# Kernel optimization log

Hardware: AMD Instinct MI355X
Metric: run time of the kernel (lower is better)

Reference implementation:

```python
import jax, jax.numpy as jnp
import numpy as np

N, E = 100000, 1600000
IN, HID, EMB = 128, 256, 64


def setup_inputs() -> dict:
    key = jax.random.key(0)
    ks = jax.random.split(key, 8)
    x = jax.random.normal(ks[0], (N, IN), dtype=jnp.float32)
    edge_index = jax.random.randint(ks[1], (2, E), 0, N, dtype=jnp.int64)
    def glorot(k, fan_in, fan_out):
        lim = np.sqrt(6.0 / (fan_in + fan_out)).astype(np.float32)
        return jax.random.uniform(k, (fan_in, fan_out), jnp.float32, -lim, lim)
    return {
        "x": x,
        "edge_index": edge_index,
        "W1": glorot(ks[2], IN, HID), "b1": jnp.zeros((HID,), jnp.float32),
        "W2": glorot(ks[3], HID, HID), "b2": jnp.zeros((HID,), jnp.float32),
        "W3": glorot(ks[4], HID, EMB), "b3": jnp.zeros((EMB,), jnp.float32),
    }


def reference(x, edge_index, W1, b1, W2, b2, W3, b3):
    n = x.shape[0]
    # add self loops (PyG GCNConv default, fill_value=1)
    loops = jnp.arange(n, dtype=edge_index.dtype)
    src = jnp.concatenate([edge_index[0], loops])
    dst = jnp.concatenate([edge_index[1], loops])
    # symmetric normalization D^-1/2 A_hat D^-1/2 (degree at target)
    deg = jax.ops.segment_sum(jnp.ones_like(src, dtype=x.dtype), dst, num_segments=n)
    dinv = jnp.where(deg > 0, deg ** -0.5, 0.0)
    norm = (dinv[src] * dinv[dst])[:, None]  # [E+N, 1]

    def conv(h, W, b):
        h = h @ W                               # [N, out]
        agg = jax.ops.segment_sum(h[src] * norm, dst, num_segments=n)
        return agg + b

    h = jax.nn.relu(conv(x, W1, b1))   # dropout: identity in eval mode
    h = jax.nn.relu(conv(h, W2, b2))
    h = conv(h, W3, b3)
    # L2-normalize rows (F.normalize, eps=1e-12)
    nrm = jnp.linalg.norm(h, axis=1, keepdims=True)
    return h / jnp.maximum(nrm, 1e-12)
```

## Files before the change

kernel.cpp:

```cpp
#include <hip/hip_runtime.h>
#include <cstddef>
#include <cstdint>

constexpr int IN_F  = 128;
constexpr int HID_F = 256;
constexpr int EMB_F = 64;

typedef float  f32x4  __attribute__((ext_vector_type(4)));
typedef short  bf16x8 __attribute__((ext_vector_type(8)));
typedef unsigned short ushort_t;
typedef ushort_t u16x8 __attribute__((ext_vector_type(8)));
typedef ushort_t u16x4 __attribute__((ext_vector_type(4)));

__device__ inline float bf2f(ushort_t u) {
  union { unsigned i; float f; } c; c.i = ((unsigned)u) << 16; return c.f;
}
__device__ inline ushort_t f2bf(float f) {
  union { float f; unsigned i; } c; c.f = f;
  unsigned r = c.i + 0x7FFFu + ((c.i >> 16) & 1u);
  return (ushort_t)(r >> 16);
}

constexpr int NBKT = 512;
constexpr int CHUNK = 16384;


__global__ void k_setup(const float* __restrict__ W1, const float* __restrict__ W2,
                        const float* __restrict__ W3,
                        ushort_t* __restrict__ W1t, ushort_t* __restrict__ W2t,
                        ushort_t* __restrict__ W3t, int* __restrict__ ghist) {
  constexpr int c1 = IN_F * HID_F;
  constexpr int c2 = c1 + HID_F * HID_F;
  constexpr int c3 = c2 + HID_F * EMB_F;
  int i = blockIdx.x * blockDim.x + threadIdx.x;
  if (i < c1) {
    int k = i / HID_F, nn = i - k * HID_F;
    W1t[(size_t)nn * IN_F + k] = f2bf(W1[i]);
  } else if (i < c2) {
    int j = i - c1;
    int k = j / HID_F, nn = j - k * HID_F;
    W2t[(size_t)nn * HID_F + k] = f2bf(W2[j]);
  } else if (i < c3) {
    int j = i - c2;
    int k = j / EMB_F, nn = j - k * EMB_F;
    W3t[(size_t)nn * HID_F + k] = f2bf(W3[j]);
  } else if (i - c3 < NBKT) {
    ghist[i - c3] = 0;
  }
}


__global__ __launch_bounds__(512) void k_hist(const int* __restrict__ dst,
                                              int* __restrict__ ghist, int e) {
  __shared__ int cnt[NBKT];
  cnt[threadIdx.x] = 0;
  __syncthreads();
  int i0 = blockIdx.x * CHUNK;
  int i1 = min(e, i0 + CHUNK);
  for (int i = i0 + threadIdx.x; i < i1; i += 512)
    atomicAdd(&cnt[dst[i] >> 8], 1);
  __syncthreads();
  int c = cnt[threadIdx.x];
  if (c > 0) atomicAdd(&ghist[threadIdx.x], c);
}

__global__ __launch_bounds__(512) void k_bscan(const int* __restrict__ ghist,
                                               int* __restrict__ bstart,
                                               int* __restrict__ gcursor) {
  __shared__ int s[NBKT];
  int v = ghist[threadIdx.x];
  s[threadIdx.x] = v;
  __syncthreads();
#pragma unroll
  for (int off = 1; off < NBKT; off <<= 1) {
    int t = (threadIdx.x >= off) ? s[threadIdx.x - off] : 0;
    __syncthreads();
    s[threadIdx.x] += t;
    __syncthreads();
  }
  int ex = s[threadIdx.x] - v;
  bstart[threadIdx.x] = ex;
  gcursor[threadIdx.x] = ex;
}

__global__ __launch_bounds__(512) void k_passA(const int* __restrict__ src,
                                               const int* __restrict__ dst,
                                               int* __restrict__ gcursor,
                                               unsigned* __restrict__ staged, int e) {
  __shared__ int cnt[NBKT];
  __shared__ int base[NBKT];
  cnt[threadIdx.x] = 0;
  __syncthreads();
  int i0 = blockIdx.x * CHUNK;
  int i1 = min(e, i0 + CHUNK);
  for (int i = i0 + threadIdx.x; i < i1; i += 512)
    atomicAdd(&cnt[dst[i] >> 8], 1);
  __syncthreads();
  int c = cnt[threadIdx.x];
  base[threadIdx.x] = (c > 0) ? atomicAdd(&gcursor[threadIdx.x], c) : 0;
  cnt[threadIdx.x] = 0;
  __syncthreads();
  for (int i = i0 + threadIdx.x; i < i1; i += 512) {
    int d = dst[i];
    int b = d >> 8;
    int lp = atomicAdd(&cnt[b], 1);
    staged[base[b] + lp] = ((unsigned)(d & 255) << 17) | (unsigned)src[i];
  }
}

__global__ __launch_bounds__(256) void k_B1scan(const unsigned* __restrict__ staged,
                                                const int* __restrict__ bstart,
                                                const int* __restrict__ ghist,
                                                float* __restrict__ dinv,
                                                int* __restrict__ rowptr,
                                                int* __restrict__ bsum, int n) {
  __shared__ int cnt[256];
  __shared__ int s[256];
  cnt[threadIdx.x] = 0;
  __syncthreads();
  int b = blockIdx.x;
  int beg = bstart[b], end = beg + ghist[b];
  for (int i = beg + threadIdx.x; i < end; i += 256)
    atomicAdd(&cnt[staged[i] >> 17], 1);
  __syncthreads();
  int node = (b << 8) + threadIdx.x;
  int v = (node < n) ? cnt[threadIdx.x] : 0;
  if (node < n) dinv[node] = rsqrtf((float)(v + 1));
  s[threadIdx.x] = v;
  __syncthreads();
#pragma unroll
  for (int off = 1; off < 256; off <<= 1) {
    int t = (threadIdx.x >= off) ? s[threadIdx.x - off] : 0;
    __syncthreads();
    s[threadIdx.x] += t;
    __syncthreads();
  }
  if (node < n) rowptr[node] = s[threadIdx.x] - v;
  if (threadIdx.x == 255) bsum[b] = s[255];
}

__global__ void k_scan2(int* __restrict__ bsum, int nb) {
  __shared__ int s[512];
  int v = (threadIdx.x < nb) ? bsum[threadIdx.x] : 0;
  s[threadIdx.x] = v;
  __syncthreads();
#pragma unroll
  for (int off = 1; off < 512; off <<= 1) {
    int t = (threadIdx.x >= off) ? s[threadIdx.x - off] : 0;
    __syncthreads();
    s[threadIdx.x] += t;
    __syncthreads();
  }
  if (threadIdx.x < nb) bsum[threadIdx.x] = s[threadIdx.x] - v;
}

__global__ void k_scan3x(int* __restrict__ rowptr, const int* __restrict__ bsum,
                         const float* __restrict__ x, const float* __restrict__ dinv,
                         ushort_t* __restrict__ xb, int n, int e) {
  int i = blockIdx.x * blockDim.x + threadIdx.x;
  int n32 = n * 32;
  if (i < n32) {
    float s = dinv[i >> 5];
    float4 v = reinterpret_cast<const float4*>(x)[i];
    u16x4 o;
    o[0] = f2bf(v.x * s); o[1] = f2bf(v.y * s); o[2] = f2bf(v.z * s); o[3] = f2bf(v.w * s);
    reinterpret_cast<u16x4*>(xb)[i] = o;
  } else {
    int j = i - n32;
    if (j < n) rowptr[j] += bsum[j >> 8];
    else if (j == n) rowptr[n] = e;
  }
}

__global__ __launch_bounds__(256) void k_B2(const unsigned* __restrict__ staged,
                                            const int* __restrict__ bstart,
                                            const int* __restrict__ ghist,
                                            const int* __restrict__ rowptr,
                                            int* __restrict__ csr, int n) {
  __shared__ int cur[256];
  cur[threadIdx.x] = 0;
  __syncthreads();
  int b = blockIdx.x;
  int beg = bstart[b], end = beg + ghist[b];
  int nb0 = b << 8;
  for (int i = beg + threadIdx.x; i < end; i += 256) {
    unsigned p = staged[i];
    int l = (int)(p >> 17);
    int s = (int)(p & 0x1FFFFu);
    int pos = rowptr[nb0 + l] + atomicAdd(&cur[l], 1);
    csr[pos] = s;
  }
}


__global__ __launch_bounds__(256) void k_gather1(
    const ushort_t* __restrict__ t, ushort_t* __restrict__ outp,
    const int* __restrict__ rowptr, const int* __restrict__ csr, int n) {
  int wid = (blockIdx.x * blockDim.x + threadIdx.x) >> 6;
  int lane = threadIdx.x & 63;
  if (wid >= n) return;
  const int half = lane >> 5, sub = lane & 31;
  const int coff = sub * 4;
  int beg = rowptr[wid], end = rowptr[wid + 1];
  int nitems = end - beg + 1;
  float acc[4] = {};
  int i = 0;
  for (; i + 3 < nitems; i += 4) {
    int i0 = i + half, i1 = i + 2 + half;
    int r0 = (i0 == 0) ? wid : csr[beg + i0 - 1];
    int r1 = csr[beg + i1 - 1];
    u16x4 v0 = *reinterpret_cast<const u16x4*>(t + (size_t)r0 * IN_F + coff);
    u16x4 v1 = *reinterpret_cast<const u16x4*>(t + (size_t)r1 * IN_F + coff);
#pragma unroll
    for (int k = 0; k < 4; ++k) acc[k] += bf2f(v0[k]);
#pragma unroll
    for (int k = 0; k < 4; ++k) acc[k] += bf2f(v1[k]);
  }
  for (; i < nitems; i += 2) {
    int i0 = i + half;
    if (i0 < nitems) {
      int r0 = (i0 == 0) ? wid : csr[beg + i0 - 1];
      u16x4 v0 = *reinterpret_cast<const u16x4*>(t + (size_t)r0 * IN_F + coff);
#pragma unroll
      for (int k = 0; k < 4; ++k) acc[k] += bf2f(v0[k]);
    }
  }
#pragma unroll
  for (int k = 0; k < 4; ++k) acc[k] += __shfl_xor(acc[k], 32);
  if (half == 0) {
    u16x4 o;
#pragma unroll
    for (int k = 0; k < 4; ++k) o[k] = f2bf(acc[k]);
    *reinterpret_cast<u16x4*>(outp + (size_t)wid * IN_F + coff) = o;
  }
}

__global__ __launch_bounds__(256) void k_gather2(
    const ushort_t* __restrict__ t, ushort_t* __restrict__ outp,
    const int* __restrict__ rowptr, const int* __restrict__ csr,
    const float* __restrict__ dinv, const float* __restrict__ bias, int n) {
  int wid = (blockIdx.x * blockDim.x + threadIdx.x) >> 6;
  int lane = threadIdx.x & 63;
  if (wid >= n) return;
  const int half = lane >> 5, sub = lane & 31;
  const int coff = sub * 8;
  int beg = rowptr[wid], end = rowptr[wid + 1];
  int nitems = end - beg + 1;
  float acc[8] = {};
  int i = 0;
  for (; i + 3 < nitems; i += 4) {
    int i0 = i + half, i1 = i + 2 + half;
    int r0 = (i0 == 0) ? wid : csr[beg + i0 - 1];
    int r1 = csr[beg + i1 - 1];
    u16x8 v0 = *reinterpret_cast<const u16x8*>(t + (size_t)r0 * HID_F + coff);
    u16x8 v1 = *reinterpret_cast<const u16x8*>(t + (size_t)r1 * HID_F + coff);
#pragma unroll
    for (int k = 0; k < 8; ++k) acc[k] += bf2f(v0[k]);
#pragma unroll
    for (int k = 0; k < 8; ++k) acc[k] += bf2f(v1[k]);
  }
  for (; i < nitems; i += 2) {
    int i0 = i + half;
    if (i0 < nitems) {
      int r0 = (i0 == 0) ? wid : csr[beg + i0 - 1];
      u16x8 v0 = *reinterpret_cast<const u16x8*>(t + (size_t)r0 * HID_F + coff);
#pragma unroll
      for (int k = 0; k < 8; ++k) acc[k] += bf2f(v0[k]);
    }
  }
#pragma unroll
  for (int k = 0; k < 8; ++k) acc[k] += __shfl_xor(acc[k], 32);
  if (half == 0) {
    float s = dinv[wid];
    u16x8 o;
#pragma unroll
    for (int k = 0; k < 8; ++k) o[k] = f2bf(fmaxf(fmaf(acc[k], s, bias[coff + k]), 0.f));
    *reinterpret_cast<u16x8*>(outp + (size_t)wid * HID_F + coff) = o;
  }
}

__global__ __launch_bounds__(256) void k_gather3(
    const ushort_t* __restrict__ t, float* __restrict__ outp,
    const int* __restrict__ rowptr, const int* __restrict__ csr,
    const float* __restrict__ dinv, const float* __restrict__ b3, int n) {
  int wid = (blockIdx.x * blockDim.x + threadIdx.x) >> 6;
  int lane = threadIdx.x & 63;
  if (wid >= n) return;
  const int q = lane >> 4, sub = lane & 15;
  const int coff = sub * 4;
  int beg = rowptr[wid], end = rowptr[wid + 1];
  int nitems = end - beg + 1;
  float acc[4] = {};
  for (int i = 0; i < nitems; i += 4) {
    int i0 = i + q;
    if (i0 < nitems) {
      int r0 = (i0 == 0) ? wid : csr[beg + i0 - 1];
      u16x4 v0 = *reinterpret_cast<const u16x4*>(t + (size_t)r0 * EMB_F + coff);
#pragma unroll
      for (int k = 0; k < 4; ++k) acc[k] += bf2f(v0[k]);
    }
  }
#pragma unroll
  for (int k = 0; k < 4; ++k) acc[k] += __shfl_xor(acc[k], 16);
#pragma unroll
  for (int k = 0; k < 4; ++k) acc[k] += __shfl_xor(acc[k], 32);
  float s = dinv[wid];
  float v[4], ss = 0.f;
#pragma unroll
  for (int k = 0; k < 4; ++k) {
    v[k] = fmaf(acc[k], s, b3[coff + k]);
    ss = fmaf(v[k], v[k], ss);
  }
#pragma unroll
  for (int off = 8; off > 0; off >>= 1) ss += __shfl_xor(ss, off);
  float inv = 1.0f / fmaxf(sqrtf(ss), 1e-12f);
  if (lane < 16) {
    float4 o = make_float4(v[0] * inv, v[1] * inv, v[2] * inv, v[3] * inv);
    *reinterpret_cast<float4*>(outp + (size_t)wid * EMB_F + coff) = o;
  }
}


template<int K, bool RELU>
__global__ __launch_bounds__(256) void k_mfma_gemm(
    const ushort_t* __restrict__ A, const ushort_t* __restrict__ Wt,
    ushort_t* __restrict__ C,
    const float* __restrict__ dinv, const float* __restrict__ bias,
    int M, int NT ) {
  int w = blockIdx.x * 4 + (threadIdx.x >> 6);
  int lane = threadIdx.x & 63;
  int mt = w / NT, nt = w - mt * NT;
  int mbase = mt * 64, nbase = nt * 64;
  if (mbase >= M) return;
  const int lrow = lane & 15;
  const int lk = (lane >> 4) * 8;
  const int N = NT * 64;

  int rows[4];
#pragma unroll
  for (int i = 0; i < 4; ++i) {
    int r = mbase + i * 16 + lrow;
    rows[i] = (r < M) ? r : (M - 1);
  }

  f32x4 acc[4][4] = {};

#pragma unroll 2
  for (int k0 = 0; k0 < K; k0 += 32) {
    bf16x8 a[4], b[4];
#pragma unroll
    for (int i = 0; i < 4; ++i)
      a[i] = *reinterpret_cast<const bf16x8*>(A + (size_t)rows[i] * K + k0 + lk);
#pragma unroll
    for (int n = 0; n < 4; ++n)
      b[n] = *reinterpret_cast<const bf16x8*>(Wt + (size_t)(nbase + n * 16 + lrow) * K + k0 + lk);
#pragma unroll
    for (int i = 0; i < 4; ++i)
#pragma unroll
      for (int n = 0; n < 4; ++n)
        acc[i][n] = __builtin_amdgcn_mfma_f32_16x16x32_bf16(a[i], b[n], acc[i][n], 0, 0, 0);
  }

#pragma unroll
  for (int i = 0; i < 4; ++i) {
    int growb = mbase + i * 16 + (lane >> 4) * 4;
#pragma unroll
    for (int r = 0; r < 4; ++r) {
      int grow = growb + r;
      if (grow >= M) continue;
      float s = dinv[grow];
#pragma unroll
      for (int n = 0; n < 4; ++n) {
        int gcol = nbase + n * 16 + (lane & 15);
        float v = acc[i][n][r] * s;
        if (RELU) v = fmaxf(v + bias[gcol], 0.f);
        C[(size_t)grow * N + gcol] = f2bf(v);
      }
    }
  }
}


extern "C" void kernel_launch(void* const* d_in, const int* in_sizes, int n_in,
                              void* d_out, int out_size, void* d_ws, size_t ws_size,
                              hipStream_t stream) {
  const float* x  = (const float*)d_in[0];
  const int*   ei = (const int*)d_in[1];
  const float* W1 = (const float*)d_in[2];
  const float* b1 = (const float*)d_in[3];
  const float* W2 = (const float*)d_in[4];
  const float* b2 = (const float*)d_in[5];
  const float* W3 = (const float*)d_in[6];
  const float* b3 = (const float*)d_in[7];
  const int N = in_sizes[0] / IN_F;
  const int E = in_sizes[1] / 2;
  const int* src = ei;
  const int* dst = ei + E;

  char* m = (char*)d_ws;
  auto alloc = [&](size_t bytes) { char* p = m; m += (bytes + 255) & ~(size_t)255; return p; };
  ushort_t* U1  = (ushort_t*)alloc((size_t)N * HID_F * 2);
  ushort_t* U2  = (ushort_t*)alloc((size_t)N * HID_F * 2);
  ushort_t* W1t = (ushort_t*)alloc((size_t)IN_F * HID_F * 2);
  ushort_t* W2t = (ushort_t*)alloc((size_t)HID_F * HID_F * 2);
  ushort_t* W3t = (ushort_t*)alloc((size_t)HID_F * EMB_F * 2);
  float*    dinv    = (float*)alloc((size_t)N * 4);
  int*      rowptr  = (int*)alloc((size_t)(N + 1) * 4);
  int*      bsum    = (int*)alloc(512 * 4);
  int*      ghist   = (int*)alloc(NBKT * 4);
  int*      bstart  = (int*)alloc(NBKT * 4);
  int*      gcursor = (int*)alloc(NBKT * 4);
  unsigned* staged  = (unsigned*)alloc((size_t)E * 4);
  int*      csr     = (int*)alloc((size_t)E * 4);
  float*    out     = (float*)d_out;

  const int nb = (N + 255) / 256;
  const int echunks = (E + CHUNK - 1) / CHUNK;
  constexpr int SETUP_W = IN_F * HID_F + HID_F * HID_F + HID_F * EMB_F + NBKT;

  k_setup<<<(SETUP_W + 255) / 256, 256, 0, stream>>>(W1, W2, W3, W1t, W2t, W3t, ghist);

  k_hist  <<<echunks, 512, 0, stream>>>(dst, ghist, E);
  k_bscan <<<1, NBKT, 0, stream>>>(ghist, bstart, gcursor);
  k_passA <<<echunks, 512, 0, stream>>>(src, dst, gcursor, staged, E);
  k_B1scan<<<nb, 256, 0, stream>>>(staged, bstart, ghist, dinv, rowptr, bsum, N);
  k_scan2 <<<1, 512, 0, stream>>>(bsum, nb);

  ushort_t* xb = U2;
  k_scan3x<<<((N * 32) + N + 1 + 255) / 256, 256, 0, stream>>>(rowptr, bsum, x, dinv, xb, N, E);

  k_B2<<<nb, 256, 0, stream>>>(staged, bstart, ghist, rowptr, csr, N);

  const int gblocks = (N + 3) / 4;
  const int MT = (N + 63) / 64;

  ushort_t* aggX = U1;
  k_gather1<<<gblocks, 256, 0, stream>>>(xb, aggX, rowptr, csr, N);
  ushort_t* h1 = U2;
  k_mfma_gemm<IN_F, true><<<(MT * (HID_F / 64) + 3) / 4, 256, 0, stream>>>(
      aggX, W1t, h1, dinv, b1, N, HID_F / 64);

  ushort_t* t2 = U1;
  k_mfma_gemm<HID_F, false><<<(MT * (HID_F / 64) + 3) / 4, 256, 0, stream>>>(
      h1, W2t, t2, dinv, nullptr, N, HID_F / 64);
  ushort_t* h2 = U2;
  k_gather2<<<gblocks, 256, 0, stream>>>(t2, h2, rowptr, csr, dinv, b2, N);

  ushort_t* t3 = U1;
  k_mfma_gemm<HID_F, false><<<(MT * (EMB_F / 64) + 3) / 4, 256, 0, stream>>>(
      h2, W3t, t3, dinv, nullptr, N, EMB_F / 64);
  k_gather3<<<gblocks, 256, 0, stream>>>(t3, out, rowptr, csr, dinv, b3, N);
}
```

Baseline: 469.4 us.

## Fuse CSR row-pointer scan, CSR fill and x prescale into one per-bucket kernel

Replaces four kernels (per-bucket count/scan, global block-sum scan, rowptr fixup plus x scaling, CSR scatter) with a single kernel per 256-node bucket. It uses the bucket start offset from the earlier bucket scan as the global row base, so the separate block-sum scan is no longer needed. The CSR fill uses shared-memory cursors seeded with the row pointers, and each block scales and converts its own rows of x to bf16 using dinv cached in shared memory. This removes three launches and a pass over staged and rowptr. In exchange the x conversion now runs on only about 391 blocks instead of a wide grid, which may reduce its parallelism.

```diff
diff --git a/kernel.cpp b/kernel.cpp
--- a/kernel.cpp
+++ b/kernel.cpp
@@ -108,87 +108,60 @@
   }
 }
 
-__global__ __launch_bounds__(256) void k_B1scan(const unsigned* __restrict__ staged,
-                                                const int* __restrict__ bstart,
-                                                const int* __restrict__ ghist,
-                                                float* __restrict__ dinv,
-                                                int* __restrict__ rowptr,
-                                                int* __restrict__ bsum, int n) {
+__global__ __launch_bounds__(256) void k_Bfused(
+    const unsigned* __restrict__ staged, const int* __restrict__ bstart,
+    const int* __restrict__ ghist, const float* __restrict__ x,
+    float* __restrict__ dinv, int* __restrict__ rowptr, int* __restrict__ csr,
+    ushort_t* __restrict__ xb, int n, int e) {
   __shared__ int cnt[256];
   __shared__ int s[256];
-  cnt[threadIdx.x] = 0;
-  __syncthreads();
-  int b = blockIdx.x;
-  int beg = bstart[b], end = beg + ghist[b];
-  for (int i = beg + threadIdx.x; i < end; i += 256)
+  __shared__ int cur[256];
+  __shared__ float dinvL[256];
+  const int tid = threadIdx.x;
+  const int b = blockIdx.x;
+  cnt[tid] = 0;
+  __syncthreads();
+  const int beg = bstart[b], end = beg + ghist[b];
+  for (int i = beg + tid; i < end; i += 256)
     atomicAdd(&cnt[staged[i] >> 17], 1);
   __syncthreads();
-  int node = (b << 8) + threadIdx.x;
-  int v = (node < n) ? cnt[threadIdx.x] : 0;
-  if (node < n) dinv[node] = rsqrtf((float)(v + 1));
-  s[threadIdx.x] = v;
+  const int node = (b << 8) + tid;
+  int v = (node < n) ? cnt[tid] : 0;
+  float dv = rsqrtf((float)(v + 1));
+  if (node < n) { dinv[node] = dv; }
+  dinvL[tid] = dv;
+  s[tid] = v;
   __syncthreads();
 #pragma unroll
   for (int off = 1; off < 256; off <<= 1) {
-    int t = (threadIdx.x >= off) ? s[threadIdx.x - off] : 0;
+    int t = (tid >= off) ? s[tid - off] : 0;
     __syncthreads();
-    s[threadIdx.x] += t;
+    s[tid] += t;
     __syncthreads();
   }
-  if (node < n) rowptr[node] = s[threadIdx.x] - v;
-  if (threadIdx.x == 255) bsum[b] = s[255];
-}
-
-__global__ void k_scan2(int* __restrict__ bsum, int nb) {
-  __shared__ int s[512];
-  int v = (threadIdx.x < nb) ? bsum[threadIdx.x] : 0;
-  s[threadIdx.x] = v;
-  __syncthreads();
-#pragma unroll
-  for (int off = 1; off < 512; off <<= 1) {
-    int t = (threadIdx.x >= off) ? s[threadIdx.x - off] : 0;
-    __syncthreads();
-    s[threadIdx.x] += t;
-    __syncthreads();
-  }
-  if (threadIdx.x < nb) bsum[threadIdx.x] = s[threadIdx.x] - v;
-}
-
-__global__ void k_scan3x(int* __restrict__ rowptr, const int* __restrict__ bsum,
-                         const float* __restrict__ x, const float* __restrict__ dinv,
-                         ushort_t* __restrict__ xb, int n, int e) {
-  int i = blockIdx.x * blockDim.x + threadIdx.x;
-  int n32 = n * 32;
-  if (i < n32) {
-    float s = dinv[i >> 5];
-    float4 v = reinterpret_cast<const float4*>(x)[i];
-    u16x4 o;
-    o[0] = f2bf(v.x * s); o[1] = f2bf(v.y * s); o[2] = f2bf(v.z * s); o[3] = f2bf(v.w * s);
-    reinterpret_cast<u16x4*>(xb)[i] = o;
-  } else {
-    int j = i - n32;
-    if (j < n) rowptr[j] += bsum[j >> 8];
-    else if (j == n) rowptr[n] = e;
-  }
-}
-
-__global__ __launch_bounds__(256) void k_B2(const unsigned* __restrict__ staged,
-                                            const int* __restrict__ bstart,
-                                            const int* __restrict__ ghist,
-                                            const int* __restrict__ rowptr,
-                                            int* __restrict__ csr, int n) {
-  __shared__ int cur[256];
-  cur[threadIdx.x] = 0;
-  __syncthreads();
-  int b = blockIdx.x;
-  int beg = bstart[b], end = beg + ghist[b];
-  int nb0 = b << 8;
-  for (int i = beg + threadIdx.x; i < end; i += 256) {
+  int rp = beg + s[tid] - v;
+  if (node < n) rowptr[node] = rp;
+  if (b == 0 && tid == 0) rowptr[n] = e;
+  cur[tid] = rp;
+  __syncthreads();
+  for (int i = beg + tid; i < end; i += 256) {
     unsigned p = staged[i];
     int l = (int)(p >> 17);
-    int s = (int)(p & 0x1FFFFu);
-    int pos = rowptr[nb0 + l] + atomicAdd(&cur[l], 1);
-    csr[pos] = s;
+    int sv = (int)(p & 0x1FFFFu);
+    int pos = atomicAdd(&cur[l], 1);
+    csr[pos] = sv;
+  }
+  const int nb0 = b << 8;
+  const int rows = min(256, n - nb0);
+  const float4* xv = reinterpret_cast<const float4*>(x) + (size_t)nb0 * 32;
+  u16x4* xo = reinterpret_cast<u16x4*>(xb) + (size_t)nb0 * 32;
+  for (int j = tid; j < rows * 32; j += 256) {
+    float sc = dinvL[j >> 5];
+    float4 vv = xv[j];
+    u16x4 o;
+    o[0] = f2bf(vv.x * sc); o[1] = f2bf(vv.y * sc);
+    o[2] = f2bf(vv.z * sc); o[3] = f2bf(vv.w * sc);
+    xo[j] = o;
   }
 }
 
@@ -406,7 +379,6 @@
   ushort_t* W3t = (ushort_t*)alloc((size_t)HID_F * EMB_F * 2);
   float*    dinv    = (float*)alloc((size_t)N * 4);
   int*      rowptr  = (int*)alloc((size_t)(N + 1) * 4);
-  int*      bsum    = (int*)alloc(512 * 4);
   int*      ghist   = (int*)alloc(NBKT * 4);
   int*      bstart  = (int*)alloc(NBKT * 4);
   int*      gcursor = (int*)alloc(NBKT * 4);
@@ -423,13 +395,9 @@
   k_hist  <<<echunks, 512, 0, stream>>>(dst, ghist, E);
   k_bscan <<<1, NBKT, 0, stream>>>(ghist, bstart, gcursor);
   k_passA <<<echunks, 512, 0, stream>>>(src, dst, gcursor, staged, E);
-  k_B1scan<<<nb, 256, 0, stream>>>(staged, bstart, ghist, dinv, rowptr, bsum, N);
-  k_scan2 <<<1, 512, 0, stream>>>(bsum, nb);
 
   ushort_t* xb = U2;
-  k_scan3x<<<((N * 32) + N + 1 + 255) / 256, 256, 0, stream>>>(rowptr, bsum, x, dinv, xb, N, E);
-
-  k_B2<<<nb, 256, 0, stream>>>(staged, bstart, ghist, rowptr, csr, N);
+  k_Bfused<<<nb, 256, 0, stream>>>(staged, bstart, ghist, x, dinv, rowptr, csr, xb, N, E);
 
   const int gblocks = (N + 3) / 4;
   const int MT = (N + 63) / 64;
```

New measurement: 460.4 us. About the same (-1.9%).
